# Performance work log

Measured on AMD Instinct MI355X. Metric: run time of the kernel, lower is better.

## Reference

```python
import jax, jax.numpy as jnp
import numpy as np

# SorscherRNN constants. NOTE: AdaptationRNN.__init__ swaps the names:
# self.beta = alpha_kwarg, self.alpha = beta_kwarg. We replicate the effective math:
#   z  = v_t @ W_ih.T + h @ W_hh.T - ALPHA_KW * v_adapt
#   v_adapt = v_adapt + BETA_KW * (z_prev - v_adapt)   (z_prev is the PREVIOUS post-subtraction z)
ALPHA_KW = 0.1  # used as the subtraction coefficient (self.beta)
BETA_KW = 0.9   # used as the adaptation rate (self.alpha)
NG, NP = 4096, 512
B, T = 64, 100


def setup_inputs() -> dict:
    key = jax.random.key(0)
    ks = jax.random.split(key, 6)
    def xavier(k, shape):
        fan_out, fan_in = shape
        a = jnp.sqrt(6.0 / (fan_in + fan_out))
        return jax.random.uniform(k, shape, jnp.float32, -a, a)
    return {
        "v": jax.random.normal(ks[0], (B, T, 2), jnp.float32),
        "p0": jax.random.uniform(ks[1], (B, NP), jnp.float32),
        "W_init": xavier(ks[2], (NG, NP)),  # init_position_encoder weight [Ng, Np]
        "W_ih": xavier(ks[3], (NG, 2)),     # RNN input weight W
        "W_hh": xavier(ks[4], (NG, NG)),    # RNN recurrent weight Wh
        "W_dec": xavier(ks[5], (NP, NG)),   # decoder weight [Np, Ng]
    }


def _sorscher_forward(v, p0, W_init, W_ih, W_hh, W_dec):
    h0 = p0 @ W_init.T                       # [B, Ng]
    va0 = jnp.zeros_like(h0)
    zp0 = jnp.zeros_like(h0)

    def step(carry, v_t):
        h, va, zp = carry
        z = v_t @ W_ih.T + h @ W_hh.T        # [B, Ng]
        z = z - ALPHA_KW * va                # z -= self.beta * v (old v)
        va = va + BETA_KW * (zp - va)        # v += self.alpha * (z_prev - v)
        s = jax.nn.relu(z)
        return (s, va, z), s                 # z_prev is post-subtraction z

    v_t_first = jnp.transpose(v, (1, 0, 2))  # [T, B, 2]
    _, g = jax.lax.scan(step, (h0, va0, zp0), v_t_first)
    g = jnp.transpose(g, (1, 0, 2))          # [B, T, Ng]
    return g @ W_dec.T                       # place_preds [B, T, Np] (log_softmax=False)


def reference(v, p0, W_init, W_ih, W_hh, W_dec):
    return _sorscher_forward(v, p0, W_init, W_ih, W_hh, W_dec)
```

## Files before the change

kernel.cpp:

```cpp
#include <hip/hip_runtime.h>
#include <hip/hip_bf16.h>

#define NG 4096
#define NP 512
#define TT 100
#define NCOL 4608
#define NKS 8
#define PLANE 262144L

typedef __bf16  bf16x8 __attribute__((ext_vector_type(8)));
typedef float   f32x4  __attribute__((ext_vector_type(4)));
typedef __hip_bfloat16 bf;
typedef unsigned short u16;

#define ALPHA_BF 0.10009765625f
#define BETA_BF  0.8984375f

__device__ __forceinline__ bf16x8 ldfrag(const bf* p) {
  return *reinterpret_cast<const bf16x8*>(p);
}
__device__ __forceinline__ f32x4 mfma16(bf16x8 a, bf16x8 b, f32x4 c) {
  return __builtin_amdgcn_mfma_f32_16x16x32_bf16(a, b, c, 0, 0, 0);
}
__device__ __forceinline__ float ldin(const void* p, long i, int isf) {
  return isf ? ((const float*)p)[i] : __bfloat162float(((const bf*)p)[i]);
}
__device__ __forceinline__ float bfr(float x) {
  return __bfloat162float(__float2bfloat16(x));
}
__device__ __forceinline__ long qidx(int m, int c) {
  int kk = c >> 5, qd = (c >> 3) & 3, j = c & 7;
  int mt = m >> 4, lm = m & 15;
  return (((long)kk * 4 + mt) * 64 + (qd * 16 + lm)) * 8 + j;
}

__global__ void probe_kernel(const u16* __restrict__ w, int* __restrict__ flag) {
  int lane = threadIdx.x;
  int okall = 1, cntb = 0;
#pragma unroll
  for (int j = 0; j < 4; ++j) {
    u16 x = w[2 * (lane * 4 + j)];
    int e = (x >> 7) & 0xFF;
    int bok = (e >= 60 && e <= 126);
    int zok = (e == 0);
    okall &= (bok | zok);
    cntb += bok;
  }
  unsigned long long b1 = __ballot(okall != 0);
  unsigned long long b2 = __ballot(cntb >= 3);
  if (lane == 0)
    *flag = (b1 == ~0ull && __popcll(b2) >= 48) ? 0 : 1;
}

__global__ __launch_bounds__(256) void cvt_pack_kernel(
    const void* __restrict__ Whh, const void* __restrict__ Wdec,
    bf* __restrict__ PH, bf* __restrict__ PL,
    const int* __restrict__ flag) {
  int isf = *flag;
  long n8 = (long)NCOL * NG / 8;
  long i = (long)blockIdx.x * 256 + threadIdx.x;
  long stride = (long)gridDim.x * 256;
  for (; i < n8; i += stride) {
    int lane = (int)(i & 63);
    int kk   = (int)((i >> 6) & 127);
    int strip= (int)(i >> 13);
    int col  = strip * 16 + (lane & 15);
    int k0   = kk * 32 + (lane >> 4) * 8;
    const void* W = (col < NG) ? Whh : Wdec;
    long src = (long)((col < NG) ? col : col - NG) * NG + k0;
    if (isf) {
      const float* ps = (const float*)W + src;
      float4 x = *(const float4*)ps, y = *(const float4*)(ps + 4);
      float xs[8] = {x.x, x.y, x.z, x.w, y.x, y.y, y.z, y.w};
      bf16x8 h, l;
#pragma unroll
      for (int j = 0; j < 8; ++j) {
        bf hh = __float2bfloat16(xs[j]);
        bf ll = __float2bfloat16(xs[j] - __bfloat162float(hh));
        h[j] = *reinterpret_cast<__bf16*>(&hh);
        l[j] = *reinterpret_cast<__bf16*>(&ll);
      }
      *reinterpret_cast<bf16x8*>(PH + i * 8) = h;
      *reinterpret_cast<bf16x8*>(PL + i * 8) = l;
    } else {
      *reinterpret_cast<bf16x8*>(PH + i * 8) =
          *reinterpret_cast<const bf16x8*>((const bf*)W + src);
    }
  }
}

__global__ __launch_bounds__(256) void init_kernel(
    const void* __restrict__ p0, const void* __restrict__ Winit,
    const int* __restrict__ flag,
    bf* __restrict__ ghi, bf* __restrict__ glo,
    float* __restrict__ va, float* __restrict__ zp)
{
  int isf = *flag;
  int g = blockIdx.x * 4 + (threadIdx.x >> 6);
  int lane = threadIdx.x & 63;
  int b  = g >> 9;
  int n0 = g & 511;
  float pf[8];
  if (isf) {
    const float* pp = (const float*)p0 + (long)b * NP + lane * 8;
    float4 x = *(const float4*)pp, y = *(const float4*)(pp + 4);
    pf[0]=x.x; pf[1]=x.y; pf[2]=x.z; pf[3]=x.w;
    pf[4]=y.x; pf[5]=y.y; pf[6]=y.z; pf[7]=y.w;
  } else {
    bf16x8 a = ldfrag((const bf*)p0 + (long)b * NP + lane * 8);
#pragma unroll
    for (int j = 0; j < 8; ++j) pf[j] = (float)a[j];
  }
#pragma unroll
  for (int it = 0; it < 8; ++it) {
    int n = n0 + (it << 9);
    float acc;
    if (isf) {
      const float* pw = (const float*)Winit + (long)n * NP + lane * 8;
      float4 x = *(const float4*)pw, y = *(const float4*)(pw + 4);
      acc = pf[0]*x.x + pf[1]*x.y + pf[2]*x.z + pf[3]*x.w
          + pf[4]*y.x + pf[5]*y.y + pf[6]*y.z + pf[7]*y.w;
    } else {
      bf16x8 wv = ldfrag((const bf*)Winit + (long)n * NP + lane * 8);
      acc = 0.f;
#pragma unroll
      for (int j = 0; j < 8; ++j) acc += pf[j] * (float)wv[j];
    }
#pragma unroll
    for (int s = 32; s >= 1; s >>= 1) acc += __shfl_xor(acc, s, 64);
    if (lane == 0) {
      bf h = __float2bfloat16(acc);
      long q = qidx(b, n);
      ghi[q] = h;
      if (isf) glo[q] = __float2bfloat16(acc - __bfloat162float(h));
      long idx = (long)b * NG + n;
      va[idx] = 0.f;
      zp[idx] = 0.f;
    }
  }
}

__global__ __launch_bounds__(512, 4) void s12_kernel(
    const bf* __restrict__ Qh, const bf* __restrict__ Ql,
    bf* __restrict__ hN, bf* __restrict__ lN,
    float* __restrict__ va, float* __restrict__ zp,
    const bf* __restrict__ PH, const bf* __restrict__ PL,
    const void* __restrict__ Wih, const void* __restrict__ vin,
    const int* __restrict__ flag, int t)
{
  int strip = blockIdx.x;
  int isf = *flag;
  int tid  = threadIdx.x;
  int ks   = tid >> 6;
  int lane = tid & 63;
  int quad = lane >> 4, l16 = lane & 15;

  const bf* pB = PH + ((long)strip * 128 + ks * 16) * 512 + lane * 8;
  const bf* pA = Qh + (long)ks * 32768 + lane * 8;

  f32x4 acc0 = {0.f,0.f,0.f,0.f}, acc1 = acc0, acc2 = acc0, acc3 = acc0;
  if (isf) {
    const bf* pBl = PL + ((long)strip * 128 + ks * 16) * 512 + lane * 8;
    const bf* pAl = Ql + (long)ks * 32768 + lane * 8;
#pragma unroll 2
    for (int i = 0; i < 16; ++i) {
      bf16x8 bh = ldfrag(pB  + i * 512);
      bf16x8 bl = ldfrag(pBl + i * 512);
      const bf* ah = pA  + i * 2048;
      const bf* al = pAl + i * 2048;
      bf16x8 a0 = ldfrag(ah);
      bf16x8 a1 = ldfrag(ah + 512);
      bf16x8 a2 = ldfrag(ah + 1024);
      bf16x8 a3 = ldfrag(ah + 1536);
      bf16x8 l0 = ldfrag(al);
      bf16x8 l1 = ldfrag(al + 512);
      bf16x8 l2 = ldfrag(al + 1024);
      bf16x8 l3 = ldfrag(al + 1536);
      acc0 = mfma16(a0, bh, acc0); acc0 = mfma16(l0, bh, acc0); acc0 = mfma16(a0, bl, acc0);
      acc1 = mfma16(a1, bh, acc1); acc1 = mfma16(l1, bh, acc1); acc1 = mfma16(a1, bl, acc1);
      acc2 = mfma16(a2, bh, acc2); acc2 = mfma16(l2, bh, acc2); acc2 = mfma16(a2, bl, acc2);
      acc3 = mfma16(a3, bh, acc3); acc3 = mfma16(l3, bh, acc3); acc3 = mfma16(a3, bl, acc3);
    }
  } else {
#pragma unroll 4
    for (int i = 0; i < 16; ++i) {
      bf16x8 bh = ldfrag(pB + i * 512);
      const bf* ah = pA + i * 2048;
      acc0 = mfma16(ldfrag(ah),        bh, acc0);
      acc1 = mfma16(ldfrag(ah + 512),  bh, acc1);
      acc2 = mfma16(ldfrag(ah + 1024), bh, acc2);
      acc3 = mfma16(ldfrag(ah + 1536), bh, acc3);
    }
  }

  __shared__ float red[NKS][64][17];
#pragma unroll
  for (int mt = 0; mt < 4; ++mt) {
    f32x4 a = (mt == 0) ? acc0 : (mt == 1) ? acc1 : (mt == 2) ? acc2 : acc3;
#pragma unroll
    for (int r = 0; r < 4; ++r)
      red[ks][mt * 16 + quad * 4 + r][l16] = a[r];
  }
  __syncthreads();

#pragma unroll
  for (int half = 0; half < 2; ++half) {
    int e = half * 512 + tid;
    int m   = e >> 4;
    int c16 = e & 15;
    int c = strip * 16 + c16;
    float z = 0.f;
#pragma unroll
    for (int k2 = 0; k2 < NKS; ++k2)
      z += red[k2][m][c16];

    float w0 = ldin(Wih, 2L * c, isf);
    float w1 = ldin(Wih, 2L * c + 1, isf);
    float v0 = ldin(vin, ((long)m * TT + t) * 2, isf);
    float v1 = ldin(vin, ((long)m * TT + t) * 2 + 1, isf);
    long idx = (long)m * NG + c;
    float vao = va[idx], zpo = zp[idx];
    if (isf) {
      z += v0 * w0 + v1 * w1;
      z -= 0.1f * vao;
      va[idx] = vao + 0.9f * (zpo - vao);
      zp[idx] = z;
      float s = fmaxf(z, 0.f);
      bf sh = __float2bfloat16(s);
      long q = qidx(m, c);
      hN[q] = sh;
      lN[q] = __float2bfloat16(s - __bfloat162float(sh));
    } else {
      float zmm = bfr(z);
      float zv  = bfr(v0 * w0 + v1 * w1);
      float z0  = bfr(zmm + zv);
      float sub = bfr(ALPHA_BF * vao);
      float z1  = bfr(z0 - sub);
      float d   = bfr(zpo - vao);
      float mm  = bfr(BETA_BF * d);
      va[idx]   = bfr(vao + mm);
      zp[idx]   = z1;
      float s = fmaxf(z1, 0.f);
      long q = qidx(m, c);
      hN[q] = __float2bfloat16(s);
    }
  }
}

__global__ __launch_bounds__(512, 4) void dec_kernel(
    const bf* __restrict__ ghi, const bf* __restrict__ glo,
    const bf* __restrict__ PH, const bf* __restrict__ PL,
    const int* __restrict__ flag, void* __restrict__ out)
{
  int strip = blockIdx.x;
  int t     = blockIdx.y;
  int isf = *flag;
  int tid  = threadIdx.x;
  int ks   = tid >> 6;
  int lane = tid & 63;
  int quad = lane >> 4, l16 = lane & 15;

  const bf* Qh = ghi + (long)(t + 1) * PLANE;
  const bf* pB = PH + ((long)(256 + strip) * 128 + ks * 16) * 512 + lane * 8;
  const bf* pA = Qh + (long)ks * 32768 + lane * 8;

  f32x4 acc0 = {0.f,0.f,0.f,0.f}, acc1 = acc0, acc2 = acc0, acc3 = acc0;
  if (isf) {
    const bf* Ql = glo + (long)(t + 1) * PLANE;
    const bf* pBl = PL + ((long)(256 + strip) * 128 + ks * 16) * 512 + lane * 8;
    const bf* pAl = Ql + (long)ks * 32768 + lane * 8;
#pragma unroll 2
    for (int i = 0; i < 16; ++i) {
      bf16x8 bh = ldfrag(pB  + i * 512);
      bf16x8 bl = ldfrag(pBl + i * 512);
      const bf* ah = pA  + i * 2048;
      const bf* al = pAl + i * 2048;
      bf16x8 a0 = ldfrag(ah);
      bf16x8 a1 = ldfrag(ah + 512);
      bf16x8 a2 = ldfrag(ah + 1024);
      bf16x8 a3 = ldfrag(ah + 1536);
      bf16x8 l0 = ldfrag(al);
      bf16x8 l1 = ldfrag(al + 512);
      bf16x8 l2 = ldfrag(al + 1024);
      bf16x8 l3 = ldfrag(al + 1536);
      acc0 = mfma16(a0, bh, acc0); acc0 = mfma16(l0, bh, acc0); acc0 = mfma16(a0, bl, acc0);
      acc1 = mfma16(a1, bh, acc1); acc1 = mfma16(l1, bh, acc1); acc1 = mfma16(a1, bl, acc1);
      acc2 = mfma16(a2, bh, acc2); acc2 = mfma16(l2, bh, acc2); acc2 = mfma16(a2, bl, acc2);
      acc3 = mfma16(a3, bh, acc3); acc3 = mfma16(l3, bh, acc3); acc3 = mfma16(a3, bl, acc3);
    }
  } else {
#pragma unroll 4
    for (int i = 0; i < 16; ++i) {
      bf16x8 bh = ldfrag(pB + i * 512);
      const bf* ah = pA + i * 2048;
      acc0 = mfma16(ldfrag(ah),        bh, acc0);
      acc1 = mfma16(ldfrag(ah + 512),  bh, acc1);
      acc2 = mfma16(ldfrag(ah + 1024), bh, acc2);
      acc3 = mfma16(ldfrag(ah + 1536), bh, acc3);
    }
  }

  __shared__ float red[NKS][64][17];
#pragma unroll
  for (int mt = 0; mt < 4; ++mt) {
    f32x4 a = (mt == 0) ? acc0 : (mt == 1) ? acc1 : (mt == 2) ? acc2 : acc3;
#pragma unroll
    for (int r = 0; r < 4; ++r)
      red[ks][mt * 16 + quad * 4 + r][l16] = a[r];
  }
  __syncthreads();

#pragma unroll
  for (int half = 0; half < 2; ++half) {
    int e = half * 512 + tid;
    int m   = e >> 4;
    int c16 = e & 15;
    float z = 0.f;
#pragma unroll
    for (int k2 = 0; k2 < NKS; ++k2)
      z += red[k2][m][c16];
    long o = ((long)m * TT + t) * NP + strip * 16 + c16;
    if (isf) ((float*)out)[o] = z;
    else     ((bf*)out)[o]    = __float2bfloat16(z);
  }
}

extern "C" void kernel_launch(void* const* d_in, const int* in_sizes, int n_in,
                              void* d_out, int out_size, void* d_ws, size_t ws_size,
                              hipStream_t stream) {
  const void* v     = d_in[0];
  const void* p0    = d_in[1];
  const void* Winit = d_in[2];
  const void* Wih   = d_in[3];
  const void* Whh   = d_in[4];
  const void* Wdec  = d_in[5];

  size_t off = 0;
  char* w = (char*)d_ws;
  int*   flag = (int*)(w + off);          off += 64;
  bf*    PH   = (bf*)(w + off);           off += (size_t)NCOL * NG * 2;
  bf*    PL   = (bf*)(w + off);           off += (size_t)NCOL * NG * 2;
  bf*    ghi  = (bf*)(w + off);           off += (size_t)(TT + 1) * PLANE * 2;
  bf*    glo  = (bf*)(w + off);           off += (size_t)(TT + 1) * PLANE * 2;
  float* va   = (float*)(w + off);        off += (size_t)64 * NG * 4;
  float* zp   = (float*)(w + off);        off += (size_t)64 * NG * 4;

  if (ws_size < off) return;

  probe_kernel<<<1, 64, 0, stream>>>((const u16*)Whh, flag);
  cvt_pack_kernel<<<9216, 256, 0, stream>>>(Whh, Wdec, PH, PL, flag);
  init_kernel<<<8192, 256, 0, stream>>>(p0, Winit, flag, ghi, glo, va, zp);

  for (int t = 0; t < TT; ++t) {
    s12_kernel<<<256, 512, 0, stream>>>(ghi + (long)t * PLANE,
                                        glo + (long)t * PLANE,
                                        ghi + (long)(t + 1) * PLANE,
                                        glo + (long)(t + 1) * PLANE,
                                        va, zp, PH, PL, Wih, v, flag, t);
  }
  dec_kernel<<<dim3(32, TT), 512, 0, stream>>>(ghi, glo, PH, PL, flag, d_out);
}
```

Before: 2.585 ms.

## Split recurrent step blocks across batch halves and reorder decoder grid

The per-timestep recurrent kernel now launches 512 blocks, each covering one 16-column strip and half of the 64-row batch, so each block does half the MFMA work and uses a smaller reduction buffer. The aim is to fill more of the CUs and shorten the critical path of each of the 100 serialized step launches. The cost is that the W_hh strip is loaded twice, once per batch half. The decoder grid is also transposed to put time on x, padded to 104 with an early return, which changes block scheduling order and L2 reuse of the weight strips.

```diff
diff --git a/kernel.cpp b/kernel.cpp
--- a/kernel.cpp
+++ b/kernel.cpp
@@ -148,7 +148,8 @@
     const void* __restrict__ Wih, const void* __restrict__ vin,
     const int* __restrict__ flag, int t)
 {
-  int strip = blockIdx.x;
+  int strip = blockIdx.x & 255;
+  int mh    = blockIdx.x >> 8;
   int isf = *flag;
   int tid  = threadIdx.x;
   int ks   = tid >> 6;
@@ -156,63 +157,50 @@
   int quad = lane >> 4, l16 = lane & 15;
 
   const bf* pB = PH + ((long)strip * 128 + ks * 16) * 512 + lane * 8;
-  const bf* pA = Qh + (long)ks * 32768 + lane * 8;
-
-  f32x4 acc0 = {0.f,0.f,0.f,0.f}, acc1 = acc0, acc2 = acc0, acc3 = acc0;
+  const bf* pA = Qh + (long)ks * 32768 + mh * 1024 + lane * 8;
+
+  f32x4 acc0 = {0.f,0.f,0.f,0.f}, acc1 = acc0;
   if (isf) {
     const bf* pBl = PL + ((long)strip * 128 + ks * 16) * 512 + lane * 8;
-    const bf* pAl = Ql + (long)ks * 32768 + lane * 8;
+    const bf* pAl = Ql + (long)ks * 32768 + mh * 1024 + lane * 8;
 #pragma unroll 2
     for (int i = 0; i < 16; ++i) {
       bf16x8 bh = ldfrag(pB  + i * 512);
       bf16x8 bl = ldfrag(pBl + i * 512);
       const bf* ah = pA  + i * 2048;
       const bf* al = pAl + i * 2048;
-      bf16x8 a0 = ldfrag(ah);
-      bf16x8 a1 = ldfrag(ah + 512);
-      bf16x8 a2 = ldfrag(ah + 1024);
-      bf16x8 a3 = ldfrag(ah + 1536);
-      bf16x8 l0 = ldfrag(al);
-      bf16x8 l1 = ldfrag(al + 512);
-      bf16x8 l2 = ldfrag(al + 1024);
-      bf16x8 l3 = ldfrag(al + 1536);
+      bf16x8 a0 = ldfrag(ah),      a1 = ldfrag(ah + 512);
+      bf16x8 l0 = ldfrag(al),      l1 = ldfrag(al + 512);
       acc0 = mfma16(a0, bh, acc0); acc0 = mfma16(l0, bh, acc0); acc0 = mfma16(a0, bl, acc0);
       acc1 = mfma16(a1, bh, acc1); acc1 = mfma16(l1, bh, acc1); acc1 = mfma16(a1, bl, acc1);
-      acc2 = mfma16(a2, bh, acc2); acc2 = mfma16(l2, bh, acc2); acc2 = mfma16(a2, bl, acc2);
-      acc3 = mfma16(a3, bh, acc3); acc3 = mfma16(l3, bh, acc3); acc3 = mfma16(a3, bl, acc3);
     }
   } else {
 #pragma unroll 4
     for (int i = 0; i < 16; ++i) {
       bf16x8 bh = ldfrag(pB + i * 512);
       const bf* ah = pA + i * 2048;
-      acc0 = mfma16(ldfrag(ah),        bh, acc0);
-      acc1 = mfma16(ldfrag(ah + 512),  bh, acc1);
-      acc2 = mfma16(ldfrag(ah + 1024), bh, acc2);
-      acc3 = mfma16(ldfrag(ah + 1536), bh, acc3);
-    }
-  }
-
-  __shared__ float red[NKS][64][17];
-#pragma unroll
-  for (int mt = 0; mt < 4; ++mt) {
-    f32x4 a = (mt == 0) ? acc0 : (mt == 1) ? acc1 : (mt == 2) ? acc2 : acc3;
-#pragma unroll
-    for (int r = 0; r < 4; ++r)
-      red[ks][mt * 16 + quad * 4 + r][l16] = a[r];
+      acc0 = mfma16(ldfrag(ah),       bh, acc0);
+      acc1 = mfma16(ldfrag(ah + 512), bh, acc1);
+    }
+  }
+
+  __shared__ float red[NKS][32][17];
+#pragma unroll
+  for (int r = 0; r < 4; ++r) {
+    red[ks][quad * 4 + r][l16]      = acc0[r];
+    red[ks][16 + quad * 4 + r][l16] = acc1[r];
   }
   __syncthreads();
 
-#pragma unroll
-  for (int half = 0; half < 2; ++half) {
-    int e = half * 512 + tid;
-    int m   = e >> 4;
-    int c16 = e & 15;
+  {
+    int ml  = tid >> 4;
+    int c16 = tid & 15;
+    int m = mh * 32 + ml;
     int c = strip * 16 + c16;
     float z = 0.f;
 #pragma unroll
     for (int k2 = 0; k2 < NKS; ++k2)
-      z += red[k2][m][c16];
+      z += red[k2][ml][c16];
 
     float w0 = ldin(Wih, 2L * c, isf);
     float w1 = ldin(Wih, 2L * c + 1, isf);
@@ -252,8 +240,9 @@
     const bf* __restrict__ PH, const bf* __restrict__ PL,
     const int* __restrict__ flag, void* __restrict__ out)
 {
-  int strip = blockIdx.x;
-  int t     = blockIdx.y;
+  int t     = blockIdx.x;
+  int strip = blockIdx.y;
+  if (t >= TT) return;
   int isf = *flag;
   int tid  = threadIdx.x;
   int ks   = tid >> 6;
@@ -352,11 +341,11 @@
   init_kernel<<<8192, 256, 0, stream>>>(p0, Winit, flag, ghi, glo, va, zp);
 
   for (int t = 0; t < TT; ++t) {
-    s12_kernel<<<256, 512, 0, stream>>>(ghi + (long)t * PLANE,
+    s12_kernel<<<512, 512, 0, stream>>>(ghi + (long)t * PLANE,
                                         glo + (long)t * PLANE,
                                         ghi + (long)(t + 1) * PLANE,
                                         glo + (long)(t + 1) * PLANE,
                                         va, zp, PH, PL, Wih, v, flag, t);
   }
-  dec_kernel<<<dim3(32, TT), 512, 0, stream>>>(ghi, glo, PH, PL, flag, d_out);
-}
+  dec_kernel<<<dim3(104, 32), 512, 0, stream>>>(ghi, glo, PH, PL, flag, d_out);
+}
```

Measured after the change: 2.810 ms. 8.7% more time.
